# Optimization experiments

Measured on AMD Instinct MI355X. Metric: run time of the kernel, lower is better.

Reference implementation:

```python
import jax, jax.numpy as jnp
import numpy as np

BS, NQ, DIMS = 4, 6400, 256
NH, NL, NP, NQUEUE = 8, 1, 4, 2


def ms_deform_attn(value, shapes_np, starts_np, loc, attn):
    # value: [B, Nv, H, D]; loc: [B, Nq, H, L, P, 2] in [0,1]; attn: [B, Nq, H, L, P]
    B, Nv, H, D = value.shape
    _, Nq, _, L, P, _ = loc.shape
    out = jnp.zeros((B, H, Nq, D), loc.dtype)
    for l in range(L):
        Hl, Wl = int(shapes_np[l, 0]), int(shapes_np[l, 1])
        s = int(starts_np[l])
        vl = value[:, s:s + Hl * Wl].transpose(0, 2, 1, 3)  # [B,H,HW,D]
        # grid_sample align_corners=False pixel coords
        x = loc[:, :, :, l, :, 0] * Wl - 0.5  # [B,Nq,H,P]
        y = loc[:, :, :, l, :, 1] * Hl - 0.5
        x0 = jnp.floor(x); y0 = jnp.floor(y)
        dx = x - x0; dy = y - y0
        x0i = x0.astype(jnp.int32); y0i = y0.astype(jnp.int32)
        acc = jnp.zeros((B, H, Nq * P, D), loc.dtype)
        corners = [(x0i, y0i, (1 - dx) * (1 - dy)),
                   (x0i + 1, y0i, dx * (1 - dy)),
                   (x0i, y0i + 1, (1 - dx) * dy),
                   (x0i + 1, y0i + 1, dx * dy)]
        for xi, yi, w in corners:
            valid = (xi >= 0) & (xi < Wl) & (yi >= 0) & (yi < Hl)
            idx = jnp.clip(yi, 0, Hl - 1) * Wl + jnp.clip(xi, 0, Wl - 1)  # [B,Nq,H,P]
            idx_t = idx.transpose(0, 2, 1, 3).reshape(B, H, Nq * P, 1)
            g = jnp.take_along_axis(vl, idx_t, axis=2)  # [B,H,Nq*P,D]
            wv = jnp.where(valid, w, 0.0).transpose(0, 2, 1, 3).reshape(B, H, Nq * P, 1)
            acc = acc + g * wv
        acc = acc.reshape(B, H, Nq, P, D)
        wl = attn[:, :, :, l].transpose(0, 2, 1, 3)  # [B,H,Nq,P]
        out = out + jnp.einsum('bhnpd,bhnp->bhnd', acc, wl)
    return out.transpose(0, 2, 1, 3).reshape(B, Nq, H * D)


def setup_inputs() -> dict:
    key = jax.random.key(0)
    ks = jax.random.split(key, 12)
    d2 = DIMS * NQUEUE
    noff = NQUEUE * NH * NL * NP * 2
    nattn = NQUEUE * NH * NL * NP
    sc = 1.0 / np.sqrt(DIMS)
    return {
        'query': jax.random.normal(ks[0], (BS, NQ, DIMS), jnp.float32),
        'voxbev': jax.random.normal(ks[1], (BS, NQ, DIMS), jnp.float32),
        'reference_points': jax.random.uniform(ks[2], (BS * NQUEUE, NQ, NL, 2), jnp.float32),
        'spatial_shapes': jnp.array([[80, 80]], dtype=jnp.int64),
        'level_start_index': jnp.array([0], dtype=jnp.int64),
        'Wv': jax.random.normal(ks[3], (DIMS, DIMS), jnp.float32) * sc,
        'bv': jax.random.normal(ks[4], (DIMS,), jnp.float32) * 0.01,
        'Woff': jax.random.normal(ks[5], (d2, noff), jnp.float32) * (1.0 / np.sqrt(d2)),
        'boff': jax.random.normal(ks[6], (noff,), jnp.float32),
        'Wattn': jax.random.normal(ks[7], (d2, nattn), jnp.float32) * (1.0 / np.sqrt(d2)),
        'battn': jax.random.normal(ks[8], (nattn,), jnp.float32) * 0.01,
        'Wo': jax.random.normal(ks[9], (DIMS, DIMS), jnp.float32) * sc,
        'bo': jax.random.normal(ks[10], (DIMS,), jnp.float32) * 0.01,
    }


def reference(query, voxbev, reference_points, spatial_shapes, level_start_index,
              Wv, bv, Woff, boff, Wattn, battn, Wo, bo):
    bs, nq, dims = query.shape
    shapes_np = np.asarray(spatial_shapes)
    starts_np = np.asarray(level_start_index)
    identity = query
    # value = stack([query, voxbev], 1).reshape(bs*2, nq, dims) -> interleaved [q0,v0,q1,v1,...]
    value = jnp.stack([query, voxbev], 1).reshape(bs * NQUEUE, nq, dims)
    qcat = jnp.concatenate([value[:bs], query], -1)  # [bs, nq, 2*dims]
    v = (value @ Wv + bv).reshape(bs * NQUEUE, nq, NH, dims // NH)
    off = (qcat @ Woff + boff).reshape(bs, nq, NH, NQUEUE, NL, NP, 2)
    attn = (qcat @ Wattn + battn).reshape(bs, nq, NH, NQUEUE, NL * NP)
    attn = jax.nn.softmax(attn, axis=-1).reshape(bs, nq, NH, NQUEUE, NL, NP)
    attn = attn.transpose(0, 3, 1, 2, 4, 5).reshape(bs * NQUEUE, nq, NH, NL, NP)
    off = off.transpose(0, 3, 1, 2, 4, 5, 6).reshape(bs * NQUEUE, nq, NH, NL, NP, 2)
    # offset normalizer: (W, H) per level
    norm = jnp.stack([spatial_shapes[:, 1], spatial_shapes[:, 0]], -1).astype(off.dtype)  # [L,2]
    loc = reference_points[:, :, None, :, None, :] + off / norm[None, None, None, :, None, :]
    out = ms_deform_attn(v, shapes_np, starts_np, loc, attn)  # [bs*2, nq, dims]
    out = out.reshape(bs, NQUEUE, nq, dims).mean(1)  # mean over queue
    out = out @ Wo + bo
    return out + identity  # dropout is identity in eval
```

## Files before the change

### kernel.cpp

```cpp
#include <hip/hip_runtime.h>
#include <hip/hip_bf16.h>

#define BS   4
#define NQ   6400
#define DIMS 256
#define NH   8
#define NP   4
#define GW   80
#define GH   80

typedef __hip_bfloat16 bf16;
typedef unsigned short ushort;
typedef __attribute__((ext_vector_type(8))) short short8;
typedef __attribute__((ext_vector_type(4))) float floatx4;

union bfu { bf16 h; ushort s; };
__device__ __forceinline__ ushort f2bs(float x) { bfu u; u.h = __float2bfloat16(x); return u.s; }
__device__ __forceinline__ float bs2f(ushort s) { return __uint_as_float(((unsigned)s) << 16); }
__device__ __forceinline__ float ldin(const void* p, size_t i, int isf) {
    return isf ? ((const float*)p)[i] : bs2f(((const ushort*)p)[i]);
}

__device__ __forceinline__ int self_detect(const ushort* __restrict__ q, int tid) {
    int bad = 0;
    const uint4 u0 = ((const uint4*)q)[tid * 2];
    const uint4 u1 = ((const uint4*)q)[tid * 2 + 1];
    const unsigned w[8] = { u0.x, u0.y, u0.z, u0.w, u1.x, u1.y, u1.z, u1.w };
    #pragma unroll
    for (int j = 0; j < 8; ++j) {
        if (((w[j] >> 7)  & 0xFF) > 160) bad = 1;
        if (((w[j] >> 23) & 0xFF) > 160) bad = 1;
    }
    return __any(bad) ? 1 : 0;
}

__global__ __launch_bounds__(256) void prep_k(
    const void* __restrict__ Wv, const void* __restrict__ bv,
    const void* __restrict__ Woff, const void* __restrict__ boff,
    const void* __restrict__ Wattn, const void* __restrict__ battn,
    const void* __restrict__ Wo, const void* __restrict__ bo,
    int* __restrict__ flagp,
    ushort* __restrict__ WvT, ushort* __restrict__ WoaT, ushort* __restrict__ WoT,
    float* __restrict__ biasv, float* __restrict__ biasoa, float* __restrict__ biaso,
    const void* __restrict__ query, const void* __restrict__ voxbev,
    uint4* __restrict__ qb, uint4* __restrict__ vbv)
{
    const int tid = threadIdx.x;
    const int isf = self_detect((const ushort*)query, tid);
    const int bid = blockIdx.x;
    if (bid == 0 && tid == 0) *flagp = isf;
    if (bid < 899) {
        const int i = bid * 256 + tid;
        const int n1 = 256 * 256, n2 = n1 + 192 * 512, n3 = n2 + 256 * 256;
        const int n4 = n3 + 256, n5 = n4 + 192, n6 = n5 + 256;
        if (i < n1) {
            int n = i >> 8, k = i & 255;
            WvT[i] = f2bs(ldin(Wv, (size_t)k * 256 + n, isf));
        } else if (i < n2) {
            int j = i - n1, n = j >> 9, k = j & 511;
            float v = (n < 128) ? ldin(Woff, (size_t)k * 128 + n, isf)
                                : ldin(Wattn, (size_t)k * 64 + (n - 128), isf);
            WoaT[j] = f2bs(v);
        } else if (i < n3) {
            int j = i - n2, n = j >> 8, k = j & 255;
            WoT[j] = f2bs(ldin(Wo, (size_t)k * 256 + n, isf));
        } else if (i < n4) {
            biasv[i - n3] = ldin(bv, i - n3, isf);
        } else if (i < n5) {
            int j = i - n4;
            biasoa[j] = (j < 128) ? ldin(boff, j, isf) : ldin(battn, j - 128, isf);
        } else if (i < n6) {
            biaso[i - n5] = ldin(bo, i - n5, isf);
        }
    } else {
        if (isf == 0) return;
        const int t = (bid - 899) * 256 + tid;
        const int half = 819200;
        const void* src = (t < half) ? query : voxbev;
        uint4* dst = (t < half) ? qb : vbv;
        const int j = (t < half) ? t : t - half;
        const float4* s = (const float4*)src + (size_t)j * 2;
        float4 a = s[0], b = s[1];
        uint4 o;
        o.x = ((unsigned)f2bs(a.y) << 16) | f2bs(a.x);
        o.y = ((unsigned)f2bs(a.w) << 16) | f2bs(a.z);
        o.z = ((unsigned)f2bs(b.y) << 16) | f2bs(b.x);
        o.w = ((unsigned)f2bs(b.w) << 16) | f2bs(b.z);
        dst[j] = o;
    }
}

enum { A_VAL = 0, A_QCAT = 1, A_PLAIN = 2 };
enum { O_BF16 = 0, O_FINAL = 1, O_VPERM = 2, O_OAPERM = 3 };

#define SROW 264
#define CST  67
#define SMEMB (128 * CST * 4)

template <int AMODE, int OMODE, int KTOT, int NX, int MG>
__device__ __forceinline__ void pgemm_body(
    const int F, char* smem,
    const ushort* __restrict__ Apl, const ushort* __restrict__ BT,
    const float* __restrict__ biasf, void* __restrict__ C,
    const void* __restrict__ query_raw, const void* __restrict__ voxbev_raw,
    const ushort* __restrict__ qb, const ushort* __restrict__ vbv,
    const int isf)
{
    constexpr int N = NX * 64;
    constexpr int NPH = KTOT / 256;
    short* pan = (short*)smem;
    float* cbf = (float*)smem;

    const int xcd = F & 7, l = F >> 3;
    const int n = l % NX;
    const int mg = (l / NX) * 8 + xcd;
    if (mg >= MG) return;
    const int bm = mg * 256, bn = n * 64;

    const int tid = threadIdx.x;
    const int lane = tid & 63, wv = tid >> 6;
    const int wm = wv * 64;
    const int fr = lane & 15, fq = (lane >> 4) * 8;

    const ushort* qsrc = isf ? qb  : (const ushort*)query_raw;
    const ushort* vsrc = isf ? vbv : (const ushort*)voxbev_raw;
    const ushort* aph[NPH];
    if (AMODE == A_PLAIN) {
        aph[0] = Apl + (size_t)bm * DIMS;
    } else {
        const int b = bm / NQ, q0 = bm - (bm / NQ) * NQ;
        aph[0] = ((b & 1) ? vsrc : qsrc) + (size_t)((b >> 1) * NQ + q0) * DIMS;
        if (AMODE == A_QCAT) aph[1] = qsrc + (size_t)(b * NQ + q0) * DIMS;
    }

    floatx4 acc[4][4] = {};

    for (int ph = 0; ph < NPH; ++ph) {
        if (ph > 0) __syncthreads();
        #pragma unroll
        for (int i = 0; i < 8; ++i) {
            const int c = tid * 8 + i;
            const int row = c >> 5, j = (c & 31) * 8;
            *(uint4*)&pan[row * SROW + j] =
                *(const uint4*)&BT[(size_t)(bn + row) * KTOT + ph * 256 + j];
        }
        __syncthreads();

        const ushort* ab = aph[ph];
        #pragma unroll
        for (int k0 = 0; k0 < 256; k0 += 32) {
            short8 af[4], bf[4];
            #pragma unroll
            for (int mt = 0; mt < 4; ++mt)
                af[mt] = *(const short8*)&ab[(size_t)(wm + mt * 16 + fr) * DIMS + k0 + fq];
            #pragma unroll
            for (int nt = 0; nt < 4; ++nt)
                bf[nt] = *(const short8*)&pan[(nt * 16 + fr) * SROW + k0 + fq];
            #pragma unroll
            for (int mt = 0; mt < 4; ++mt)
                #pragma unroll
                for (int nt = 0; nt < 4; ++nt)
                    acc[mt][nt] = __builtin_amdgcn_mfma_f32_16x16x32_bf16(
                        af[mt], bf[nt], acc[mt][nt], 0, 0, 0);
        }
    }

    const int col = lane & 15, rq = (lane >> 4) * 4;
    const int lbase = wm & 127;
    #pragma unroll
    for (int half = 0; half < 2; ++half) {
        __syncthreads();
        if ((wv >> 1) == half) {
            #pragma unroll
            for (int mt = 0; mt < 4; ++mt)
                #pragma unroll
                for (int nt = 0; nt < 4; ++nt)
                    #pragma unroll
                    for (int r = 0; r < 4; ++r)
                        cbf[(lbase + mt * 16 + rq + r) * CST + nt * 16 + col] =
                            acc[mt][nt][r];
        }
        __syncthreads();

        if (OMODE == O_FINAL && isf) {
            const int r16 = tid >> 4, cc = tid & 15;
            #pragma unroll
            for (int it = 0; it < 8; ++it) {
                const int lr = it * 16 + r16;
                const size_t g = (size_t)(bm + half * 128 + lr);
                float4 x = *(const float4*)&cbf[lr * CST + cc * 4];
                const ushort* rs = qsrc + g * DIMS + bn + cc * 4;
                x.x += biasf[bn + cc * 4 + 0] + bs2f(rs[0]);
                x.y += biasf[bn + cc * 4 + 1] + bs2f(rs[1]);
                x.z += biasf[bn + cc * 4 + 2] + bs2f(rs[2]);
                x.w += biasf[bn + cc * 4 + 3] + bs2f(rs[3]);
                *(float4*)((float*)C + g * N + bn + cc * 4) = x;
            }
        } else {
            const int r8 = tid >> 3, c8 = tid & 7;
            #pragma unroll
            for (int it = 0; it < 4; ++it) {
                const int lr = it * 32 + r8;
                const size_t g = (size_t)(bm + half * 128 + lr);
                float4 x0 = *(const float4*)&cbf[lr * CST + c8 * 8];
                float4 x1 = *(const float4*)&cbf[lr * CST + c8 * 8 + 4];
                float xs[8] = { x0.x, x0.y, x0.z, x0.w, x1.x, x1.y, x1.z, x1.w };
                #pragma unroll
                for (int e = 0; e < 8; ++e) xs[e] += biasf[bn + c8 * 8 + e];
                if (OMODE == O_FINAL) {
                    const ushort* rs = qsrc + g * DIMS + bn + c8 * 8;
                    #pragma unroll
                    for (int e = 0; e < 8; ++e) xs[e] += bs2f(rs[e]);
                }
                uint4 o;
                o.x = ((unsigned)f2bs(xs[1]) << 16) | f2bs(xs[0]);
                o.y = ((unsigned)f2bs(xs[3]) << 16) | f2bs(xs[2]);
                o.z = ((unsigned)f2bs(xs[5]) << 16) | f2bs(xs[4]);
                o.w = ((unsigned)f2bs(xs[7]) << 16) | f2bs(xs[6]);
                ushort* dstp;
                if (OMODE == O_VPERM) {
                    const int cc = bn + c8 * 8;
                    const int s = (int)(g / NQ), qq = (int)(g % NQ);
                    dstp = (ushort*)C + ((size_t)(s * 8 + (cc >> 5)) * NQ + qq) * 32
                                      + (cc & 31);
                } else if (OMODE == O_OAPERM) {
                    const int cc = bn + c8 * 8;
                    const int bb = (int)(g / NQ), qq = (int)(g % NQ);
                    int hh, off;
                    if (cc < 128) { hh = cc >> 4; off = cc & 15; }
                    else          { hh = (cc - 128) >> 3; off = 16; }
                    dstp = (ushort*)C + ((size_t)(bb * 8 + hh) * NQ + qq) * 24 + off;
                } else {
                    dstp = (ushort*)C + g * N + bn + c8 * 8;
                }
                *(uint4*)dstp = o;
            }
        }
    }
}

__global__ __launch_bounds__(256) void gemm12_k(
    const ushort* __restrict__ WvT, const float* __restrict__ biasv,
    ushort* __restrict__ v_ws,
    const ushort* __restrict__ WoaT, const float* __restrict__ biasoa,
    ushort* __restrict__ offraw,
    const void* __restrict__ query_raw, const void* __restrict__ voxbev_raw,
    const ushort* __restrict__ qb, const ushort* __restrict__ vbv,
    const int* __restrict__ flagp)
{
    __shared__ __align__(16) char smem[SMEMB];
    const int isf = *flagp;
    const int bid = blockIdx.x;
    if (bid < 800) {
        pgemm_body<A_VAL, O_VPERM, 256, 4, 200>(bid, smem,
            nullptr, WvT, biasv, (void*)v_ws, query_raw, voxbev_raw, qb, vbv, isf);
    } else {
        pgemm_body<A_QCAT, O_OAPERM, 512, 3, 100>(bid - 800, smem,
            nullptr, WoaT, biasoa, (void*)offraw, query_raw, voxbev_raw, qb, vbv, isf);
    }
}

__global__ __launch_bounds__(256) void gemm4_k(
    const ushort* __restrict__ Apl, const ushort* __restrict__ BT,
    const float* __restrict__ biasf, void* __restrict__ C,
    const void* __restrict__ query_raw, const void* __restrict__ voxbev_raw,
    const ushort* __restrict__ qb, const ushort* __restrict__ vbv,
    const int* __restrict__ flagp)
{
    __shared__ __align__(16) char smem[SMEMB];
    const int isf = *flagp;
    pgemm_body<A_PLAIN, O_FINAL, 256, 4, 100>(blockIdx.x, smem,
        Apl, BT, biasf, C, query_raw, voxbev_raw, qb, vbv, isf);
}

__global__ __launch_bounds__(256) void sample_k(
    const ushort* __restrict__ v,
    const ushort* __restrict__ offp,
    const void* __restrict__ refpts,
    const int* __restrict__ flagp,
    ushort* __restrict__ sampled)
{
    const int isf = *flagp;
    __shared__ int   sidx[64][2][17];
    __shared__ float swt [64][2][17];
    const int tid = threadIdx.x;
    const int j = blockIdx.x;
    const int h = j & 7;
    const int k = j >> 3;
    const int b = k / 100;
    const int q0 = (k % 100) * 64;

    if (tid < 128) {
        const int lq = tid >> 1, queue = tid & 1;
        const int q = q0 + lq;
        const ushort* rec = offp + ((size_t)(b * 8 + h) * NQ + q) * 24;
        const ushort* al = rec + 16 + queue * 4;
        float l0 = bs2f(al[0]), l1 = bs2f(al[1]), l2 = bs2f(al[2]), l3 = bs2f(al[3]);
        float mx = fmaxf(fmaxf(l0, l1), fmaxf(l2, l3));
        float e0 = __expf(l0 - mx), e1 = __expf(l1 - mx);
        float e2 = __expf(l2 - mx), e3 = __expf(l3 - mx);
        float inv = 0.5f / (e0 + e1 + e2 + e3);
        const int bq = b * 2 + queue;
        const float rx = ldin(refpts, ((size_t)bq * NQ + q) * 2 + 0, isf);
        const float ry = ldin(refpts, ((size_t)bq * NQ + q) * 2 + 1, isf);
        const ushort* od = rec + queue * 8;
        float ww[4] = { e0 * inv, e1 * inv, e2 * inv, e3 * inv };
        #pragma unroll
        for (int p = 0; p < NP; ++p) {
            const float x = rx * (float)GW + bs2f(od[p * 2 + 0]) - 0.5f;
            const float y = ry * (float)GH + bs2f(od[p * 2 + 1]) - 0.5f;
            const float x0f = floorf(x), y0f = floorf(y);
            const float dx = x - x0f, dy = y - y0f;
            const int x0 = (int)x0f, y0 = (int)y0f;
            const float wp = ww[p];
            const float cw4[4] = { wp * (1.0f - dx) * (1.0f - dy),
                                   wp * dx * (1.0f - dy),
                                   wp * (1.0f - dx) * dy,
                                   wp * dx * dy };
            #pragma unroll
            for (int c = 0; c < 4; ++c) {
                const int xs = x0 + (c & 1), ys = y0 + (c >> 1);
                const bool ok = (unsigned)xs < (unsigned)GW && (unsigned)ys < (unsigned)GH;
                const int xi = min(max(xs, 0), GW - 1);
                const int yi = min(max(ys, 0), GH - 1);
                sidx[lq][queue][p * 4 + c] = yi * GW + xi;
                swt [lq][queue][p * 4 + c] = ok ? cw4[c] : 0.0f;
            }
        }
    }
    __syncthreads();

    const int lq = tid >> 2, d8 = tid & 3;
    const int q = q0 + lq;
    float a[8] = {};
    #pragma unroll
    for (int queue = 0; queue < 2; ++queue) {
        const ushort* vb = v + (((size_t)(b * 2 + queue) * 8 + h) * NQ) * 32 + d8 * 8;
        #pragma unroll
        for (int hf = 0; hf < 2; ++hf) {
            uint4 g[8];
            #pragma unroll
            for (int u = 0; u < 8; ++u) {
                const int ci = sidx[lq][queue][hf * 8 + u];
                g[u] = *(const uint4*)&vb[(size_t)ci * 32];
            }
            __builtin_amdgcn_sched_barrier(0);
            #pragma unroll
            for (int u = 0; u < 8; ++u) {
                const float cw = swt[lq][queue][hf * 8 + u];
                a[0] += cw * bs2f((ushort)g[u].x); a[1] += cw * bs2f((ushort)(g[u].x >> 16));
                a[2] += cw * bs2f((ushort)g[u].y); a[3] += cw * bs2f((ushort)(g[u].y >> 16));
                a[4] += cw * bs2f((ushort)g[u].z); a[5] += cw * bs2f((ushort)(g[u].z >> 16));
                a[6] += cw * bs2f((ushort)g[u].w); a[7] += cw * bs2f((ushort)(g[u].w >> 16));
            }
        }
    }
    uint4 o;
    o.x = ((unsigned)f2bs(a[1]) << 16) | f2bs(a[0]);
    o.y = ((unsigned)f2bs(a[3]) << 16) | f2bs(a[2]);
    o.z = ((unsigned)f2bs(a[5]) << 16) | f2bs(a[4]);
    o.w = ((unsigned)f2bs(a[7]) << 16) | f2bs(a[6]);
    *(uint4*)&sampled[((size_t)b * NQ + q) * DIMS + h * 32 + d8 * 8] = o;
}

extern "C" void kernel_launch(void* const* d_in, const int* in_sizes, int n_in,
                              void* d_out, int out_size, void* d_ws, size_t ws_size,
                              hipStream_t stream)
{
    const void* query  = d_in[0];
    const void* voxbev = d_in[1];
    const void* refpts = d_in[2];
    const void* Wv   = d_in[5];  const void* bv    = d_in[6];
    const void* Woff = d_in[7];  const void* boff  = d_in[8];
    const void* Wattn= d_in[9];  const void* battn = d_in[10];
    const void* Wo   = d_in[11]; const void* bo    = d_in[12];

    char* p = (char*)d_ws;
    int* flag = (int*)p;             p += 256;
    ushort* WvT  = (ushort*)p;       p += 256 * 256 * 2;
    ushort* WoaT = (ushort*)p;       p += 192 * 512 * 2;
    ushort* WoT  = (ushort*)p;       p += 256 * 256 * 2;
    float* biasv  = (float*)p;       p += 1024;
    float* biasoa = (float*)p;       p += 1024;
    float* biaso  = (float*)p;       p += 1024;
    ushort* qb   = (ushort*)p;       p += (size_t)BS * NQ * DIMS * 2;
    ushort* vbv  = (ushort*)p;       p += (size_t)BS * NQ * DIMS * 2;
    ushort* v_ws = (ushort*)p;       p += (size_t)2 * BS * NQ * DIMS * 2;
    ushort* offraw = (ushort*)p;     p += (size_t)BS * NQ * 192 * 2;
    ushort* sampled = (ushort*)p;

    prep_k<<<7299, 256, 0, stream>>>(Wv, bv, Woff, boff, Wattn, battn, Wo, bo,
                                     flag, WvT, WoaT, WoT, biasv, biasoa, biaso,
                                     query, voxbev, (uint4*)qb, (uint4*)vbv);

    gemm12_k<<<1112, 256, 0, stream>>>(WvT, biasv, v_ws, WoaT, biasoa, offraw,
                                       query, voxbev, qb, vbv, flag);

    sample_k<<<3200, 256, 0, stream>>>(v_ws, offraw, refpts, flag, sampled);

    gemm4_k<<<416, 256, 0, stream>>>(sampled, WoT, biaso, d_out,
                                     query, voxbev, qb, vbv, flag);
}
```

Baseline: 203.5 us.

## Halve GEMM M-tile and stage A through double-buffered LDS

The shared GEMM body now uses 128-row M tiles instead of 256, with each wave computing 32 rows, which doubles the grid sizes of both GEMM launches. A tiles are no longer read straight from global memory into MFMA fragments. They are staged in 32-wide K chunks through two padded LDS buffers, and the next chunk is prefetched while the current one feeds the MFMAs. The goal is more blocks for occupancy and coalesced A loads with overlapped latency. The cost is a __syncthreads per K step and a B panel that is reloaded twice as often relative to compute.

```diff
diff --git a/kernel.cpp b/kernel.cpp
--- a/kernel.cpp
+++ b/kernel.cpp
@@ -94,8 +94,9 @@
 enum { O_BF16 = 0, O_FINAL = 1, O_VPERM = 2, O_OAPERM = 3 };
 
 #define SROW 264
+#define APAD 40
 #define CST  67
-#define SMEMB (128 * CST * 4)
+#define SMEMB (64 * SROW * 2 + 2 * 128 * APAD * 2)
 
 template <int AMODE, int OMODE, int KTOT, int NX, int MG>
 __device__ __forceinline__ void pgemm_body(
@@ -109,18 +110,21 @@
     constexpr int N = NX * 64;
     constexpr int NPH = KTOT / 256;
     short* pan = (short*)smem;
+    short* ap0 = (short*)(smem + 64 * SROW * 2);
+    short* ap1 = ap0 + 128 * APAD;
     float* cbf = (float*)smem;
 
     const int xcd = F & 7, l = F >> 3;
     const int n = l % NX;
     const int mg = (l / NX) * 8 + xcd;
     if (mg >= MG) return;
-    const int bm = mg * 256, bn = n * 64;
+    const int bm = mg * 128, bn = n * 64;
 
     const int tid = threadIdx.x;
     const int lane = tid & 63, wv = tid >> 6;
-    const int wm = wv * 64;
+    const int wm = wv * 32;
     const int fr = lane & 15, fq = (lane >> 4) * 8;
+    const int arow = tid >> 1, acs = (tid & 1) * 16;
 
     const ushort* qsrc = isf ? qb  : (const ushort*)query_raw;
     const ushort* vsrc = isf ? vbv : (const ushort*)voxbev_raw;
@@ -133,10 +137,9 @@
         if (AMODE == A_QCAT) aph[1] = qsrc + (size_t)(b * NQ + q0) * DIMS;
     }
 
-    floatx4 acc[4][4] = {};
+    floatx4 acc[2][4] = {};
 
     for (int ph = 0; ph < NPH; ++ph) {
-        if (ph > 0) __syncthreads();
         #pragma unroll
         for (int i = 0; i < 8; ++i) {
             const int c = tid * 8 + i;
@@ -144,97 +147,107 @@
             *(uint4*)&pan[row * SROW + j] =
                 *(const uint4*)&BT[(size_t)(bn + row) * KTOT + ph * 256 + j];
         }
+        const ushort* ab = aph[ph];
+        {
+            uint4 s0 = *(const uint4*)&ab[(size_t)arow * DIMS + acs];
+            uint4 s1 = *(const uint4*)&ab[(size_t)arow * DIMS + acs + 8];
+            *(uint4*)&ap0[arow * APAD + acs] = s0;
+            *(uint4*)&ap0[arow * APAD + acs + 8] = s1;
+        }
         __syncthreads();
 
-        const ushort* ab = aph[ph];
-        #pragma unroll
-        for (int k0 = 0; k0 < 256; k0 += 32) {
-            short8 af[4], bf[4];
-            #pragma unroll
-            for (int mt = 0; mt < 4; ++mt)
-                af[mt] = *(const short8*)&ab[(size_t)(wm + mt * 16 + fr) * DIMS + k0 + fq];
+        #pragma unroll
+        for (int t = 0; t < 8; ++t) {
+            const short* acur = (t & 1) ? ap1 : ap0;
+            short* anxt = (t & 1) ? ap0 : ap1;
+            uint4 s0, s1;
+            if (t < 7) {
+                s0 = *(const uint4*)&ab[(size_t)arow * DIMS + (t + 1) * 32 + acs];
+                s1 = *(const uint4*)&ab[(size_t)arow * DIMS + (t + 1) * 32 + acs + 8];
+            }
+            short8 af[2], bf[4];
+            #pragma unroll
+            for (int mt = 0; mt < 2; ++mt)
+                af[mt] = *(const short8*)&acur[(wm + mt * 16 + fr) * APAD + fq];
             #pragma unroll
             for (int nt = 0; nt < 4; ++nt)
-                bf[nt] = *(const short8*)&pan[(nt * 16 + fr) * SROW + k0 + fq];
-            #pragma unroll
-            for (int mt = 0; mt < 4; ++mt)
+                bf[nt] = *(const short8*)&pan[(nt * 16 + fr) * SROW + t * 32 + fq];
+            #pragma unroll
+            for (int mt = 0; mt < 2; ++mt)
                 #pragma unroll
                 for (int nt = 0; nt < 4; ++nt)
                     acc[mt][nt] = __builtin_amdgcn_mfma_f32_16x16x32_bf16(
                         af[mt], bf[nt], acc[mt][nt], 0, 0, 0);
+            if (t < 7) {
+                *(uint4*)&anxt[arow * APAD + acs] = s0;
+                *(uint4*)&anxt[arow * APAD + acs + 8] = s1;
+            }
+            __syncthreads();
         }
     }
 
     const int col = lane & 15, rq = (lane >> 4) * 4;
-    const int lbase = wm & 127;
     #pragma unroll
-    for (int half = 0; half < 2; ++half) {
-        __syncthreads();
-        if ((wv >> 1) == half) {
-            #pragma unroll
-            for (int mt = 0; mt < 4; ++mt)
+    for (int mt = 0; mt < 2; ++mt)
+        #pragma unroll
+        for (int nt = 0; nt < 4; ++nt)
+            #pragma unroll
+            for (int r = 0; r < 4; ++r)
+                cbf[(wm + mt * 16 + rq + r) * CST + nt * 16 + col] = acc[mt][nt][r];
+    __syncthreads();
+
+    if (OMODE == O_FINAL && isf) {
+        const int r16 = tid >> 4, cc = tid & 15;
+        #pragma unroll
+        for (int it = 0; it < 8; ++it) {
+            const int lr = it * 16 + r16;
+            const size_t g = (size_t)(bm + lr);
+            float4 x = *(const float4*)&cbf[lr * CST + cc * 4];
+            const ushort* rs = qsrc + g * DIMS + bn + cc * 4;
+            x.x += biasf[bn + cc * 4 + 0] + bs2f(rs[0]);
+            x.y += biasf[bn + cc * 4 + 1] + bs2f(rs[1]);
+            x.z += biasf[bn + cc * 4 + 2] + bs2f(rs[2]);
+            x.w += biasf[bn + cc * 4 + 3] + bs2f(rs[3]);
+            *(float4*)((float*)C + g * N + bn + cc * 4) = x;
+        }
+    } else {
+        const int r8 = tid >> 3, c8 = tid & 7;
+        #pragma unroll
+        for (int it = 0; it < 4; ++it) {
+            const int lr = it * 32 + r8;
+            const size_t g = (size_t)(bm + lr);
+            float4 x0 = *(const float4*)&cbf[lr * CST + c8 * 8];
+            float4 x1 = *(const float4*)&cbf[lr * CST + c8 * 8 + 4];
+            float xs[8] = { x0.x, x0.y, x0.z, x0.w, x1.x, x1.y, x1.z, x1.w };
+            #pragma unroll
+            for (int e = 0; e < 8; ++e) xs[e] += biasf[bn + c8 * 8 + e];
+            if (OMODE == O_FINAL) {
+                const ushort* rs = qsrc + g * DIMS + bn + c8 * 8;
                 #pragma unroll
-                for (int nt = 0; nt < 4; ++nt)
-                    #pragma unroll
-                    for (int r = 0; r < 4; ++r)
-                        cbf[(lbase + mt * 16 + rq + r) * CST + nt * 16 + col] =
-                            acc[mt][nt][r];
-        }
-        __syncthreads();
-
-        if (OMODE == O_FINAL && isf) {
-            const int r16 = tid >> 4, cc = tid & 15;
-            #pragma unroll
-            for (int it = 0; it < 8; ++it) {
-                const int lr = it * 16 + r16;
-                const size_t g = (size_t)(bm + half * 128 + lr);
-                float4 x = *(const float4*)&cbf[lr * CST + cc * 4];
-                const ushort* rs = qsrc + g * DIMS + bn + cc * 4;
-                x.x += biasf[bn + cc * 4 + 0] + bs2f(rs[0]);
-                x.y += biasf[bn + cc * 4 + 1] + bs2f(rs[1]);
-                x.z += biasf[bn + cc * 4 + 2] + bs2f(rs[2]);
-                x.w += biasf[bn + cc * 4 + 3] + bs2f(rs[3]);
-                *(float4*)((float*)C + g * N + bn + cc * 4) = x;
-            }
-        } else {
-            const int r8 = tid >> 3, c8 = tid & 7;
-            #pragma unroll
-            for (int it = 0; it < 4; ++it) {
-                const int lr = it * 32 + r8;
-                const size_t g = (size_t)(bm + half * 128 + lr);
-                float4 x0 = *(const float4*)&cbf[lr * CST + c8 * 8];
-                float4 x1 = *(const float4*)&cbf[lr * CST + c8 * 8 + 4];
-                float xs[8] = { x0.x, x0.y, x0.z, x0.w, x1.x, x1.y, x1.z, x1.w };
-                #pragma unroll
-                for (int e = 0; e < 8; ++e) xs[e] += biasf[bn + c8 * 8 + e];
-                if (OMODE == O_FINAL) {
-                    const ushort* rs = qsrc + g * DIMS + bn + c8 * 8;
-                    #pragma unroll
-                    for (int e = 0; e < 8; ++e) xs[e] += bs2f(rs[e]);
-                }
-                uint4 o;
-                o.x = ((unsigned)f2bs(xs[1]) << 16) | f2bs(xs[0]);
-                o.y = ((unsigned)f2bs(xs[3]) << 16) | f2bs(xs[2]);
-                o.z = ((unsigned)f2bs(xs[5]) << 16) | f2bs(xs[4]);
-                o.w = ((unsigned)f2bs(xs[7]) << 16) | f2bs(xs[6]);
-                ushort* dstp;
-                if (OMODE == O_VPERM) {
-                    const int cc = bn + c8 * 8;
-                    const int s = (int)(g / NQ), qq = (int)(g % NQ);
-                    dstp = (ushort*)C + ((size_t)(s * 8 + (cc >> 5)) * NQ + qq) * 32
-                                      + (cc & 31);
-                } else if (OMODE == O_OAPERM) {
-                    const int cc = bn + c8 * 8;
-                    const int bb = (int)(g / NQ), qq = (int)(g % NQ);
-                    int hh, off;
-                    if (cc < 128) { hh = cc >> 4; off = cc & 15; }
-                    else          { hh = (cc - 128) >> 3; off = 16; }
-                    dstp = (ushort*)C + ((size_t)(bb * 8 + hh) * NQ + qq) * 24 + off;
-                } else {
-                    dstp = (ushort*)C + g * N + bn + c8 * 8;
-                }
-                *(uint4*)dstp = o;
-            }
+                for (int e = 0; e < 8; ++e) xs[e] += bs2f(rs[e]);
+            }
+            uint4 o;
+            o.x = ((unsigned)f2bs(xs[1]) << 16) | f2bs(xs[0]);
+            o.y = ((unsigned)f2bs(xs[3]) << 16) | f2bs(xs[2]);
+            o.z = ((unsigned)f2bs(xs[5]) << 16) | f2bs(xs[4]);
+            o.w = ((unsigned)f2bs(xs[7]) << 16) | f2bs(xs[6]);
+            ushort* dstp;
+            if (OMODE == O_VPERM) {
+                const int cc = bn + c8 * 8;
+                const int s = (int)(g / NQ), qq = (int)(g % NQ);
+                dstp = (ushort*)C + ((size_t)(s * 8 + (cc >> 5)) * NQ + qq) * 32
+                                  + (cc & 31);
+            } else if (OMODE == O_OAPERM) {
+                const int cc = bn + c8 * 8;
+                const int bb = (int)(g / NQ), qq = (int)(g % NQ);
+                int hh, off;
+                if (cc < 128) { hh = cc >> 4; off = cc & 15; }
+                else          { hh = (cc - 128) >> 3; off = 16; }
+                dstp = (ushort*)C + ((size_t)(bb * 8 + hh) * NQ + qq) * 24 + off;
+            } else {
+                dstp = (ushort*)C + g * N + bn + c8 * 8;
+            }
+            *(uint4*)dstp = o;
         }
     }
 }
@@ -251,11 +264,11 @@
     __shared__ __align__(16) char smem[SMEMB];
     const int isf = *flagp;
     const int bid = blockIdx.x;
-    if (bid < 800) {
-        pgemm_body<A_VAL, O_VPERM, 256, 4, 200>(bid, smem,
+    if (bid < 1600) {
+        pgemm_body<A_VAL, O_VPERM, 256, 4, 400>(bid, smem,
             nullptr, WvT, biasv, (void*)v_ws, query_raw, voxbev_raw, qb, vbv, isf);
     } else {
-        pgemm_body<A_QCAT, O_OAPERM, 512, 3, 100>(bid - 800, smem,
+        pgemm_body<A_QCAT, O_OAPERM, 512, 3, 200>(bid - 1600, smem,
             nullptr, WoaT, biasoa, (void*)offraw, query_raw, voxbev_raw, qb, vbv, isf);
     }
 }
@@ -269,7 +282,7 @@
 {
     __shared__ __align__(16) char smem[SMEMB];
     const int isf = *flagp;
-    pgemm_body<A_PLAIN, O_FINAL, 256, 4, 100>(blockIdx.x, smem,
+    pgemm_body<A_PLAIN, O_FINAL, 256, 4, 200>(blockIdx.x, smem,
         Apl, BT, biasf, C, query_raw, voxbev_raw, qb, vbv, isf);
 }
 
@@ -393,11 +406,11 @@
                                      flag, WvT, WoaT, WoT, biasv, biasoa, biaso,
                                      query, voxbev, (uint4*)qb, (uint4*)vbv);
 
-    gemm12_k<<<1112, 256, 0, stream>>>(WvT, biasv, v_ws, WoaT, biasoa, offraw,
+    gemm12_k<<<2200, 256, 0, stream>>>(WvT, biasv, v_ws, WoaT, biasoa, offraw,
                                        query, voxbev, qb, vbv, flag);
 
     sample_k<<<3200, 256, 0, stream>>>(v_ws, offraw, refpts, flag, sampled);
 
-    gemm4_k<<<416, 256, 0, stream>>>(sampled, WoT, biaso, d_out,
+    gemm4_k<<<800, 256, 0, stream>>>(sampled, WoT, biaso, d_out,
                                      query, voxbev, qb, vbv, flag);
 }
```

Result: slower. 209.7 us (+3.1%).
